# Kernel optimization log

Measured on AMD Instinct MI355X. Metric: run time of the kernel, lower is better.

The kernel has to match this reference:

```python
import jax, jax.numpy as jnp
import numpy as np

V, E, H = 32000, 128, 128

def setup_inputs() -> dict:
    key = jax.random.key(0)
    ks = jax.random.split(key, 12)
    s = 0.05
    x = jax.random.randint(ks[0], (256, 512), 0, V)
    emb = jax.random.normal(ks[1], (V, E), jnp.float32) * s
    Wi = jax.random.normal(ks[2], (E + H, H), jnp.float32) * s
    bi = jnp.zeros((H,), jnp.float32)
    Wf = jax.random.normal(ks[3], (E + H, H), jnp.float32) * s
    bf = jnp.zeros((H,), jnp.float32)
    Wc = jax.random.normal(ks[4], (E + H, H), jnp.float32) * s
    bc = jnp.zeros((H,), jnp.float32)
    Wo = jax.random.normal(ks[5], (E + H, H), jnp.float32) * s
    bo = jnp.zeros((H,), jnp.float32)
    Wout = jax.random.normal(ks[6], (H, V), jnp.float32) * s
    bout = jnp.zeros((V,), jnp.float32)
    return {"x": x, "emb": emb, "Wi": Wi, "bi": bi, "Wf": Wf, "bf": bf,
            "Wc": Wc, "bc": bc, "Wo": Wo, "bo": bo, "Wout": Wout, "bout": bout}

def reference(x, emb, Wi, bi, Wf, bf, Wc, bc, Wo, bo, Wout, bout):
    B, T = x.shape
    xe = emb[x]                       # [B, T, E] embedding gather
    xe_t = jnp.swapaxes(xe, 0, 1)     # [T, B, E] for scan over time

    def step(carry, e_t):
        h, c = carry
        comb = jnp.concatenate([e_t, h], axis=1)          # [B, E+H]
        f = jax.nn.sigmoid(comb @ Wf + bf)
        i = jax.nn.sigmoid(comb @ Wi + bi)
        o = jax.nn.sigmoid(comb @ Wo + bo)
        c_ = jnp.tanh(comb @ Wc + bc)
        c = f * c + i * c_
        h = o * jnp.tanh(c)
        return (h, c), None

    h0 = jnp.zeros((B, H), xe.dtype)
    c0 = jnp.zeros((B, H), xe.dtype)
    (h, _), _ = jax.lax.scan(step, (h0, c0), xe_t)
    return h @ Wout + bout            # [B, V] logits from final hidden state
```

## Files before the change

### kernel.cpp

```cpp
#include <hip/hip_runtime.h>

constexpr int TT = 512;
constexpr int BB = 256;
constexpr int HH = 128;
constexpr int VV = 32000;

typedef _Float16 h2 __attribute__((ext_vector_type(2)));
typedef _Float16 f16x4 __attribute__((ext_vector_type(4)));
typedef _Float16 f16x8 __attribute__((ext_vector_type(8)));
typedef float f32x4 __attribute__((ext_vector_type(4)));

struct __align__(16) H2x4 { h2 a, b, c, d; };

__device__ __forceinline__ h2 pkrtz(float a, float b) {
  return __builtin_bit_cast(h2, __builtin_amdgcn_cvt_pkrtz(a, b));
}
__device__ __forceinline__ float fexp2(float x) {
  return __builtin_amdgcn_exp2f(x);
}
__device__ __forceinline__ float frcp(float x) {
  return __builtin_amdgcn_rcpf(x);
}

constexpr float SC_SIG = -1.4426950408889634f;
constexpr float SC_TANH = 2.8853900817779268f;

__global__ __launch_bounds__(256, 4) void wprep(
    const float* __restrict__ Wi, const float* __restrict__ bi,
    const float* __restrict__ Wf, const float* __restrict__ bf,
    const float* __restrict__ Wc, const float* __restrict__ bc,
    const float* __restrict__ Wo, const float* __restrict__ bo,
    _Float16* __restrict__ Wct, float* __restrict__ bcat) {
  const int n = blockIdx.x;
  const int g = n & 3;
  const int u = n >> 2;
  const float* Wg = (g == 0) ? Wi : (g == 1) ? Wf : (g == 2) ? Wc : Wo;
  const float* bg = (g == 0) ? bi : (g == 1) ? bf : (g == 2) ? bc : bo;
  const float sc = (g == 2) ? SC_TANH : SC_SIG;
  const int k = threadIdx.x;
  Wct[(size_t)n * 256 + k] = (_Float16)(Wg[(size_t)k * HH + u] * sc);
  if (k == 0) bcat[n] = bg[u] * sc;
}

__global__ __launch_bounds__(512, 2) void lstm_rec(
    const int* __restrict__ x, const float* __restrict__ emb,
    const _Float16* __restrict__ Wct, const float* __restrict__ bcat,
    _Float16* __restrict__ hbf) {
  const int b = blockIdx.x;
  const int tid = threadIdx.x;
  const int w = tid >> 6;
  const int l = tid & 63;
  const int n16 = l & 15;
  const int quad = l >> 4;
  const int nts = n16 & 3;
  const int u = 16 * w + 4 * nts + quad;

  __shared__ int xrow[TT];
  __shared__ __align__(16) _Float16 comb[2][HH];
  __shared__ __align__(16) _Float16 xch[64][516];

  xrow[tid] = x[(size_t)b * TT + tid];
  if (tid < HH) comb[0][tid] = (_Float16)0.f;

  f16x8 wh[4][4];
#pragma unroll
  for (int nt = 0; nt < 4; ++nt)
#pragma unroll
    for (int ks = 0; ks < 4; ++ks)
      wh[nt][ks] = *(const f16x8*)(Wct +
                                   (size_t)(64 * w + nt * 16 + n16) * 256 +
                                   128 + ks * 32 + quad * 8);

  f16x8 wfx[4][4];
  f32x4 biasr[4];
#pragma unroll
  for (int nt = 0; nt < 4; ++nt) {
#pragma unroll
    for (int ks = 0; ks < 4; ++ks)
      wfx[nt][ks] = *(const f16x8*)(Wct +
                                    (size_t)(64 * w + nt * 16 + n16) * 256 +
                                    ks * 32 + quad * 8);
    biasr[nt] = *(const f32x4*)(bcat + 64 * w + nt * 16 + quad * 4);
  }

  float cst = 0.f;
  float hv = 0.f;
  int buf = 0;

  __syncthreads();

  for (int c = 0; c < 8; ++c) {
#pragma unroll 2
    for (int tt = 0; tt < 4; ++tt) {
      const int vid = xrow[c * 64 + tt * 16 + n16];
      const float* ep = emb + (size_t)vid * HH + quad * 8;
      f16x8 ef[4];
#pragma unroll
      for (int ks = 0; ks < 4; ++ks) {
        const float4 e0 = *(const float4*)(ep + ks * 32);
        const float4 e1 = *(const float4*)(ep + ks * 32 + 4);
        H2x4 q;
        q.a = pkrtz(e0.x, e0.y);
        q.b = pkrtz(e0.z, e0.w);
        q.c = pkrtz(e1.x, e1.y);
        q.d = pkrtz(e1.z, e1.w);
        ef[ks] = __builtin_bit_cast(f16x8, q);
      }
      f32x4 acc[4] = {};
#pragma unroll
      for (int ks = 0; ks < 4; ++ks)
#pragma unroll
        for (int nt = 0; nt < 4; ++nt)
          acc[nt] = __builtin_amdgcn_mfma_f32_16x16x32_f16(wfx[nt][ks], ef[ks],
                                                           acc[nt], 0, 0, 0);
#pragma unroll
      for (int nt = 0; nt < 4; ++nt) {
        const f32x4 av = acc[nt] + biasr[nt];
        _Float16* dst = &xch[tt * 16 + n16][64 * w + nt * 16 + quad * 4];
        *(h2*)dst = pkrtz(av[0], av[1]);
        *(h2*)(dst + 2) = pkrtz(av[2], av[3]);
      }
    }
    __syncthreads();

#pragma unroll 2
    for (int tl = 0; tl < 64; ++tl) {
      const f16x4 xe4 = *(const f16x4*)(&xch[tl][4 * u]);

      const _Float16* cb = comb[buf];
      f16x8 hb[4];
#pragma unroll
      for (int ks = 0; ks < 4; ++ks)
        hb[ks] = *(const f16x8*)(cb + ks * 32 + quad * 8);

      f32x4 acc[4] = {};
#pragma unroll
      for (int ks = 0; ks < 4; ++ks)
#pragma unroll
        for (int nt = 0; nt < 4; ++nt)
          acc[nt] = __builtin_amdgcn_mfma_f32_16x16x32_f16(wh[nt][ks], hb[ks],
                                                           acc[nt], 0, 0, 0);

      const bool s1 = (n16 & 1) != 0;
      const bool s2 = (n16 & 2) != 0;
      const f32x4 t01 = s1 ? acc[1] : acc[0];
      const f32x4 t23 = s1 ? acc[3] : acc[2];
      const f32x4 av = s2 ? t23 : t01;

      const float a0 = av[0] + (float)xe4[0];
      const float a1 = av[1] + (float)xe4[1];
      const float a2 = av[2] + (float)xe4[2];
      const float a3 = av[3] + (float)xe4[3];

      const float ei = fexp2(a0);
      const float ef_ = fexp2(a1);
      const float ec = fexp2(a2);
      const float eo = fexp2(a3);
      const float gi = frcp(1.f + ei);
      const float gf = frcp(1.f + ef_);
      const float gc = 1.f - 2.f * frcp(1.f + ec);
      const float go = frcp(1.f + eo);
      cst = gf * cst + gi * gc;
      const float th = 1.f - 2.f * frcp(1.f + fexp2(cst * SC_TANH));
      hv = go * th;

      if (n16 < 4) comb[buf ^ 1][u] = (_Float16)hv;
      __syncthreads();
      buf ^= 1;
    }
  }
  if (n16 < 4) hbf[(size_t)b * HH + u] = (_Float16)hv;
}

__global__ __launch_bounds__(256, 4) void wout_tr(const float* __restrict__ Wout,
                                                  _Float16* __restrict__ Wt) {
  const int v = blockIdx.x * 256 + threadIdx.x;
#pragma unroll 1
  for (int kc = 0; kc < 16; ++kc) {
    float f[8];
#pragma unroll
    for (int i = 0; i < 8; ++i) f[i] = Wout[(size_t)(kc * 8 + i) * VV + v];
    H2x4 q;
    q.a = pkrtz(f[0], f[1]);
    q.b = pkrtz(f[2], f[3]);
    q.c = pkrtz(f[4], f[5]);
    q.d = pkrtz(f[6], f[7]);
    *(H2x4*)(Wt + (size_t)v * HH + kc * 8) = q;
  }
}

__global__ __launch_bounds__(256, 4) void lstm_out(
    const _Float16* __restrict__ Wt, const _Float16* __restrict__ hbf,
    const float* __restrict__ bout, float* __restrict__ out) {
  const int tid = threadIdx.x;
  const int wv = tid >> 6;
  const int lane = tid & 63;
  const int vblk = blockIdx.x % 250;
  const int batblk = blockIdx.x / 250;
  const int n16 = lane & 15;
  const int quad = lane >> 4;
  const int vbase = vblk * 128 + wv * 32;
  const int batbase = batblk * 64;

  f32x4 acc[4][2] = {};
#pragma unroll
  for (int ks = 0; ks < 4; ++ks) {
    const int k = ks * 32 + quad * 8;
    f16x8 a[4], bf_[2];
#pragma unroll
    for (int mt = 0; mt < 4; ++mt)
      a[mt] = *(const f16x8*)(hbf + (size_t)(batbase + mt * 16 + n16) * HH + k);
#pragma unroll
    for (int vt = 0; vt < 2; ++vt)
      bf_[vt] = *(const f16x8*)(Wt + (size_t)(vbase + vt * 16 + n16) * HH + k);
#pragma unroll
    for (int mt = 0; mt < 4; ++mt)
#pragma unroll
      for (int vt = 0; vt < 2; ++vt)
        acc[mt][vt] = __builtin_amdgcn_mfma_f32_16x16x32_f16(a[mt], bf_[vt],
                                                             acc[mt][vt], 0, 0, 0);
  }
#pragma unroll
  for (int vt = 0; vt < 2; ++vt) {
    const int v = vbase + vt * 16 + n16;
    const float bv = bout[v];
#pragma unroll
    for (int mt = 0; mt < 4; ++mt) {
#pragma unroll
      for (int r = 0; r < 4; ++r) {
        const int bat = batbase + mt * 16 + quad * 4 + r;
        out[(size_t)bat * VV + v] = acc[mt][vt][r] + bv;
      }
    }
  }
}

extern "C" void kernel_launch(void* const* d_in, const int* in_sizes, int n_in,
                              void* d_out, int out_size, void* d_ws,
                              size_t ws_size, hipStream_t stream) {
  const int* x = (const int*)d_in[0];
  const float* emb = (const float*)d_in[1];
  const float* Wi = (const float*)d_in[2];
  const float* bi = (const float*)d_in[3];
  const float* Wf = (const float*)d_in[4];
  const float* bf = (const float*)d_in[5];
  const float* Wc = (const float*)d_in[6];
  const float* bc = (const float*)d_in[7];
  const float* Wo = (const float*)d_in[8];
  const float* bo = (const float*)d_in[9];
  const float* Wout = (const float*)d_in[10];
  const float* bout = (const float*)d_in[11];
  float* out = (float*)d_out;

  _Float16* Wt = (_Float16*)d_ws;
  _Float16* hbf = Wt + (size_t)VV * HH;
  _Float16* Wct = hbf + (size_t)BB * HH;
  float* bcat = (float*)(Wct + 512 * 256);

  wprep<<<512, 256, 0, stream>>>(Wi, bi, Wf, bf, Wc, bc, Wo, bo, Wct, bcat);
  wout_tr<<<VV / 256, 256, 0, stream>>>(Wout, Wt);
  lstm_rec<<<BB, 512, 0, stream>>>(x, emb, Wct, bcat, hbf);
  lstm_out<<<(VV / 128) * (BB / 64), 256, 0, stream>>>(Wt, hbf, bout, out);
}
```

Baseline: 426.2 us.

## Halve recurrent block to four waves with eight gate tiles per wave

The recurrent LSTM kernel moves from 512 threads (8 waves) to 256 threads (4 waves), and each wave now owns 128 gate rows (8 MFMA tiles) instead of 64. The aim is to make the per-timestep __syncthreads cheaper and to cut barrier participants along the serial chain. Other changes: the first MFMA now starts from a zero accumulator, and the embedding-projection add goes through fdot2. The cost is twice the MFMA work per wave per step plus a much larger register footprint, since 64 f16x8 weight registers are held per lane, which could cause spills or longer per-step latency.

```diff
diff --git a/kernel.cpp b/kernel.cpp
--- a/kernel.cpp
+++ b/kernel.cpp
@@ -20,6 +20,9 @@
 }
 __device__ __forceinline__ float frcp(float x) {
   return __builtin_amdgcn_rcpf(x);
+}
+__device__ __forceinline__ float fdot2(h2 a, h2 b, float c) {
+  return __builtin_amdgcn_fdot2(a, b, c, false);
 }
 
 constexpr float SC_SIG = -1.4426950408889634f;
@@ -42,7 +45,7 @@
   if (k == 0) bcat[n] = bg[u] * sc;
 }
 
-__global__ __launch_bounds__(512, 2) void lstm_rec(
+__global__ __launch_bounds__(256, 1) void lstm_rec(
     const int* __restrict__ x, const float* __restrict__ emb,
     const _Float16* __restrict__ Wct, const float* __restrict__ bcat,
     _Float16* __restrict__ hbf) {
@@ -52,36 +55,41 @@
   const int l = tid & 63;
   const int n16 = l & 15;
   const int quad = l >> 4;
-  const int nts = n16 & 3;
-  const int u = 16 * w + 4 * nts + quad;
+  const int nts = n16 & 7;
+  const int u = 32 * w + 4 * nts + quad;
 
   __shared__ int xrow[TT];
   __shared__ __align__(16) _Float16 comb[2][HH];
   __shared__ __align__(16) _Float16 xch[64][516];
 
   xrow[tid] = x[(size_t)b * TT + tid];
+  xrow[tid + 256] = x[(size_t)b * TT + tid + 256];
   if (tid < HH) comb[0][tid] = (_Float16)0.f;
 
-  f16x8 wh[4][4];
-#pragma unroll
-  for (int nt = 0; nt < 4; ++nt)
+  f16x8 wh[8][4];
+#pragma unroll
+  for (int nt = 0; nt < 8; ++nt)
 #pragma unroll
     for (int ks = 0; ks < 4; ++ks)
       wh[nt][ks] = *(const f16x8*)(Wct +
-                                   (size_t)(64 * w + nt * 16 + n16) * 256 +
+                                   (size_t)(128 * w + nt * 16 + n16) * 256 +
                                    128 + ks * 32 + quad * 8);
 
-  f16x8 wfx[4][4];
-  f32x4 biasr[4];
-#pragma unroll
-  for (int nt = 0; nt < 4; ++nt) {
+  f16x8 wfx[8][4];
+  f32x4 biasr[8];
+#pragma unroll
+  for (int nt = 0; nt < 8; ++nt) {
 #pragma unroll
     for (int ks = 0; ks < 4; ++ks)
       wfx[nt][ks] = *(const f16x8*)(Wct +
-                                    (size_t)(64 * w + nt * 16 + n16) * 256 +
+                                    (size_t)(128 * w + nt * 16 + n16) * 256 +
                                     ks * 32 + quad * 8);
-    biasr[nt] = *(const f32x4*)(bcat + 64 * w + nt * 16 + quad * 4);
-  }
+    biasr[nt] = *(const f32x4*)(bcat + 128 * w + nt * 16 + quad * 4);
+  }
+
+  const f32x4 ZR4 = {0.f, 0.f, 0.f, 0.f};
+  const h2 E10 = h2{(_Float16)1.f, (_Float16)0.f};
+  const h2 E01 = h2{(_Float16)0.f, (_Float16)1.f};
 
   float cst = 0.f;
   float hv = 0.f;
@@ -106,17 +114,21 @@
         q.d = pkrtz(e1.z, e1.w);
         ef[ks] = __builtin_bit_cast(f16x8, q);
       }
-      f32x4 acc[4] = {};
-#pragma unroll
-      for (int ks = 0; ks < 4; ++ks)
-#pragma unroll
-        for (int nt = 0; nt < 4; ++nt)
+      f32x4 acc[8];
+#pragma unroll
+      for (int nt = 0; nt < 8; ++nt)
+        acc[nt] = __builtin_amdgcn_mfma_f32_16x16x32_f16(wfx[nt][0], ef[0],
+                                                         ZR4, 0, 0, 0);
+#pragma unroll
+      for (int ks = 1; ks < 4; ++ks)
+#pragma unroll
+        for (int nt = 0; nt < 8; ++nt)
           acc[nt] = __builtin_amdgcn_mfma_f32_16x16x32_f16(wfx[nt][ks], ef[ks],
                                                            acc[nt], 0, 0, 0);
 #pragma unroll
-      for (int nt = 0; nt < 4; ++nt) {
+      for (int nt = 0; nt < 8; ++nt) {
         const f32x4 av = acc[nt] + biasr[nt];
-        _Float16* dst = &xch[tt * 16 + n16][64 * w + nt * 16 + quad * 4];
+        _Float16* dst = &xch[tt * 16 + n16][128 * w + nt * 16 + quad * 4];
         *(h2*)dst = pkrtz(av[0], av[1]);
         *(h2*)(dst + 2) = pkrtz(av[2], av[3]);
       }
@@ -125,7 +137,9 @@
 
 #pragma unroll 2
     for (int tl = 0; tl < 64; ++tl) {
-      const f16x4 xe4 = *(const f16x4*)(&xch[tl][4 * u]);
+      const h2* xp = (const h2*)(&xch[tl][4 * u]);
+      const h2 xlo = xp[0];
+      const h2 xhi = xp[1];
 
       const _Float16* cb = comb[buf];
       f16x8 hb[4];
@@ -133,24 +147,33 @@
       for (int ks = 0; ks < 4; ++ks)
         hb[ks] = *(const f16x8*)(cb + ks * 32 + quad * 8);
 
-      f32x4 acc[4] = {};
-#pragma unroll
-      for (int ks = 0; ks < 4; ++ks)
-#pragma unroll
-        for (int nt = 0; nt < 4; ++nt)
+      f32x4 acc[8];
+#pragma unroll
+      for (int nt = 0; nt < 8; ++nt)
+        acc[nt] = __builtin_amdgcn_mfma_f32_16x16x32_f16(wh[nt][0], hb[0],
+                                                         ZR4, 0, 0, 0);
+#pragma unroll
+      for (int ks = 1; ks < 4; ++ks)
+#pragma unroll
+        for (int nt = 0; nt < 8; ++nt)
           acc[nt] = __builtin_amdgcn_mfma_f32_16x16x32_f16(wh[nt][ks], hb[ks],
                                                            acc[nt], 0, 0, 0);
 
-      const bool s1 = (n16 & 1) != 0;
-      const bool s2 = (n16 & 2) != 0;
-      const f32x4 t01 = s1 ? acc[1] : acc[0];
-      const f32x4 t23 = s1 ? acc[3] : acc[2];
-      const f32x4 av = s2 ? t23 : t01;
-
-      const float a0 = av[0] + (float)xe4[0];
-      const float a1 = av[1] + (float)xe4[1];
-      const float a2 = av[2] + (float)xe4[2];
-      const float a3 = av[3] + (float)xe4[3];
+      const bool b0 = (n16 & 1) != 0;
+      const bool b1 = (n16 & 2) != 0;
+      const bool b2 = (n16 & 4) != 0;
+      const f32x4 m0 = b2 ? acc[4] : acc[0];
+      const f32x4 m1 = b2 ? acc[5] : acc[1];
+      const f32x4 m2 = b2 ? acc[6] : acc[2];
+      const f32x4 m3 = b2 ? acc[7] : acc[3];
+      const f32x4 p0 = b1 ? m2 : m0;
+      const f32x4 p1 = b1 ? m3 : m1;
+      const f32x4 av = b0 ? p1 : p0;
+
+      const float a0 = fdot2(xlo, E10, av[0]);
+      const float a1 = fdot2(xlo, E01, av[1]);
+      const float a2 = fdot2(xhi, E10, av[2]);
+      const float a3 = fdot2(xhi, E01, av[3]);
 
       const float ei = fexp2(a0);
       const float ef_ = fexp2(a1);
@@ -164,12 +187,12 @@
       const float th = 1.f - 2.f * frcp(1.f + fexp2(cst * SC_TANH));
       hv = go * th;
 
-      if (n16 < 4) comb[buf ^ 1][u] = (_Float16)hv;
+      if (n16 < 8) comb[buf ^ 1][u] = (_Float16)hv;
       __syncthreads();
       buf ^= 1;
     }
   }
-  if (n16 < 4) hbf[(size_t)b * HH + u] = (_Float16)hv;
+  if (n16 < 8) hbf[(size_t)b * HH + u] = (_Float16)hv;
 }
 
 __global__ __launch_bounds__(256, 4) void wout_tr(const float* __restrict__ Wout,
@@ -259,6 +282,6 @@
 
   wprep<<<512, 256, 0, stream>>>(Wi, bi, Wf, bf, Wc, bc, Wo, bo, Wct, bcat);
   wout_tr<<<VV / 256, 256, 0, stream>>>(Wout, Wt);
-  lstm_rec<<<BB, 512, 0, stream>>>(x, emb, Wct, bcat, hbf);
+  lstm_rec<<<BB, 256, 0, stream>>>(x, emb, Wct, bcat, hbf);
   lstm_out<<<(VV / 128) * (BB / 64), 256, 0, stream>>>(Wt, hbf, bout, out);
 }
```

Result: slower. 502.6 us (+17.9%).
